# Kernel tuning notes

Measured on AMD Instinct MI355X. Metric: run time of the kernel, lower is better.

The kernel has to match this reference:

```python
import jax, jax.numpy as jnp
import numpy as np

N_NODES = 100000
N_EDGES = 1600000
IN_FEATS = 64
H_FEATS = 64
NUM_CLASSES = 32


def _cgnn(h, e, src, dst, W, b, n_nodes):
    # message: m = h[src] * e  (e is [E,1], broadcasts over feature dim)
    m = h[src] * e  # [E, F]
    # segment mean over destination nodes (DGL fn.mean -> 0 for isolated nodes)
    s = jax.ops.segment_sum(m, dst, num_segments=n_nodes)  # [N, F]
    deg = jax.ops.segment_sum(jnp.ones((m.shape[0],), m.dtype), dst,
                              num_segments=n_nodes)  # [N]
    h_N = s / jnp.maximum(deg, 1.0)[:, None]
    h_total = jnp.concatenate([h, h_N], axis=1)  # [N, 2F]
    return h_total @ W + b


def setup_inputs() -> dict:
    key = jax.random.key(0)
    k = jax.random.split(key, 8)
    in_feat = jax.random.normal(k[0], (N_NODES, IN_FEATS), dtype=jnp.float32)
    edge_feat = jax.random.uniform(k[1], (N_EDGES, 1), dtype=jnp.float32)
    src = jax.random.randint(k[2], (N_EDGES,), 0, N_NODES)
    dst = jax.random.randint(k[3], (N_EDGES,), 0, N_NODES)
    # Linear(2*in_feats, h_feats) and Linear(2*h_feats, num_classes)
    s1 = 1.0 / np.sqrt(2 * IN_FEATS)
    s2 = 1.0 / np.sqrt(2 * H_FEATS)
    W1 = jax.random.uniform(k[4], (2 * IN_FEATS, H_FEATS), jnp.float32, -s1, s1)
    b1 = jax.random.uniform(k[5], (H_FEATS,), jnp.float32, -s1, s1)
    W2 = jax.random.uniform(k[6], (2 * H_FEATS, NUM_CLASSES), jnp.float32, -s2, s2)
    b2 = jax.random.uniform(k[7], (NUM_CLASSES,), jnp.float32, -s2, s2)
    return {"in_feat": in_feat, "edge_feat": edge_feat, "src": src,
            "dst": dst, "W1": W1, "b1": b1, "W2": W2, "b2": b2}


def reference(in_feat, edge_feat, src, dst, W1, b1, W2, b2):
    h = _cgnn(in_feat, edge_feat, src, dst, W1, b1, N_NODES)
    h = jax.nn.relu(h)
    h = _cgnn(h, edge_feat, src, dst, W2, b2, N_NODES)
    return h
```

## Files before the change

kernel.cpp:

```cpp
#include <hip/hip_runtime.h>
#include <hip/hip_bf16.h>


#define F 64
#define EPT 8
#define TPB 1024
#define EPB (EPT * TPB)
#define SBSHIFT 8
#define SBSZ 256
#define NSBMAX 512
#define PADSB 4864

__global__ __launch_bounds__(256) void init_cursor_kernel(
    int* __restrict__ bcursor, int nsb)
{
    const int i = blockIdx.x * 256 + threadIdx.x;
    if (i < nsb) bcursor[i] = i * PADSB;
}

__global__ __launch_bounds__(TPB) void multisplit_kernel(
    const int* __restrict__ src, const int* __restrict__ dst,
    const float* __restrict__ ef, int* __restrict__ bcursor,
    int2* __restrict__ brec, int n_edges, int nsb)
{
    __shared__ int lcnt[NSBMAX];
    __shared__ int lbase[NSBMAX];
    const int tid = threadIdx.x;
    for (int i = tid; i < nsb; i += TPB) lcnt[i] = 0;
    __syncthreads();

    const int e0 = blockIdx.x * EPB + tid;
    int d[EPT], rk[EPT];
#pragma unroll
    for (int k = 0; k < EPT; ++k) {
        const int e = e0 + k * TPB;
        const int dd = (e < n_edges) ? dst[e] : -1;
        d[k]  = dd;
        rk[k] = (dd >= 0) ? atomicAdd(&lcnt[dd >> SBSHIFT], 1) : 0;
    }
    __syncthreads();
    for (int i = tid; i < nsb; i += TPB) {
        const int c = lcnt[i];
        lbase[i] = c ? atomicAdd(&bcursor[i], c) : 0;
    }
    __syncthreads();
#pragma unroll
    for (int k = 0; k < EPT; ++k) {
        const int e = e0 + k * TPB;
        if (e < n_edges) {
            const int dd  = d[k];
            const int bkt = dd >> SBSHIFT;
            const int pos = lbase[bkt] + rk[k];
            if (pos < (bkt + 1) * PADSB)
                brec[pos] = make_int2(((dd & (SBSZ - 1)) << 17) | src[e],
                                      __float_as_int(ef[e]));
        }
    }
}

__global__ __launch_bounds__(512) void bucket_sort_kernel(
    int2* __restrict__ brec, const int* __restrict__ bcursor,
    int* __restrict__ off2, int* __restrict__ end2,
    float* __restrict__ invdeg, int n_nodes)
{
    __shared__ int2 stage[PADSB];
    __shared__ int  lcnt[SBSZ];
    __shared__ int  lcur[SBSZ];
    __shared__ int  wsum[4];

    const int b   = blockIdx.x;
    const int tid = threadIdx.x;
    const int w0  = b * PADSB;
    int cnt = bcursor[b] - w0;
    if (cnt > PADSB) cnt = PADSB;

    if (tid < SBSZ) lcnt[tid] = 0;
    __syncthreads();

    for (int i = tid; i < cnt; i += 512) {
        const int2 r = brec[w0 + i];
        stage[i] = r;
        atomicAdd(&lcnt[r.x >> 17], 1);
    }
    __syncthreads();

    int v = 0, c = 0;
    if (tid < SBSZ) {
        c = lcnt[tid];
        v = c;
        for (int d = 1; d < 64; d <<= 1) {
            int t = __shfl_up(v, d, 64);
            if ((tid & 63) >= d) v += t;
        }
        if ((tid & 63) == 63) wsum[tid >> 6] = v;
    }
    __syncthreads();
    if (tid == 0) {
        int a = 0;
#pragma unroll
        for (int i = 0; i < 4; ++i) { int t = wsum[i]; wsum[i] = a; a += t; }
    }
    __syncthreads();
    if (tid < SBSZ) {
        const int excl = wsum[tid >> 6] + (v - c);
        lcur[tid] = excl;
        const int node = (b << SBSHIFT) + tid;
        if (node < n_nodes) {
            off2[node]   = w0 + excl;
            end2[node]   = w0 + excl + c;
            invdeg[node] = 1.0f / fmaxf((float)c, 1.0f);
        }
    }
    __syncthreads();

    for (int i = tid; i < cnt; i += 512) {
        const int2 r   = stage[i];
        const int  pos = atomicAdd(&lcur[r.x >> 17], 1);
        brec[w0 + pos] = make_int2((r.x & 0x1FFFF) << 7, r.y);
    }
}

__device__ __forceinline__ unsigned bf16_rne(float f)
{
    unsigned u = __float_as_uint(f);
    return (u + 0x7FFFu + ((u >> 16) & 1u)) >> 16;
}

__global__ __launch_bounds__(256) void f32_to_bf16_kernel(
    const float* __restrict__ x, unsigned short* __restrict__ y, int n8)
{
    const int i = blockIdx.x * 256 + threadIdx.x;
    if (i >= n8) return;
    const float4 a = ((const float4*)x)[2 * i];
    const float4 b = ((const float4*)x)[2 * i + 1];
    uint4 o;
    o.x = bf16_rne(a.x) | (bf16_rne(a.y) << 16);
    o.y = bf16_rne(a.z) | (bf16_rne(a.w) << 16);
    o.z = bf16_rne(b.x) | (bf16_rne(b.y) << 16);
    o.w = bf16_rne(b.z) | (bf16_rne(b.w) << 16);
    ((uint4*)y)[i] = o;
}

__global__ __launch_bounds__(256) void agg_kernel(
    const unsigned short* __restrict__ hb, const int2* __restrict__ rec,
    const int* __restrict__ off, const int* __restrict__ end,
    const float* __restrict__ invdeg, float* __restrict__ s, int n_nodes)
{
    const int wid  = (blockIdx.x * 256 + threadIdx.x) >> 6;
    const int lane = threadIdx.x & 63;
    const int n    = lane >> 5;
    const int r    = lane & 31;
    const int g    = r >> 3;
    const int q    = r & 7;

    const int  node   = wid * 2 + n;
    const bool active = node < n_nodes;
    const int  e0 = active ? off[node] : 0;
    const int  e1 = active ? end[node] : 0;

    const char* __restrict__ hq = (const char*)hb + q * 16;

    float4 aA0 = make_float4(0.f, 0.f, 0.f, 0.f);
    float4 aA1 = make_float4(0.f, 0.f, 0.f, 0.f);
    float4 aB0 = make_float4(0.f, 0.f, 0.f, 0.f);
    float4 aB1 = make_float4(0.f, 0.f, 0.f, 0.f);

    for (int base = e0; base < e1; base += 8) {
        const int  eA = base + g;
        const int  eB = base + 4 + g;
        const bool vA = eA < e1;
        const bool vB = eB < e1;
        const int2 rA = rec[vA ? eA : e0];
        const int2 rB = rec[vB ? eB : e0];
        const float evA = vA ? __int_as_float(rA.y) : 0.f;
        const float evB = vB ? __int_as_float(rB.y) : 0.f;
        const uint4 xA = *(const uint4*)(hq + rA.x);
        const uint4 xB = *(const uint4*)(hq + rB.x);

        aA0.x = fmaf(__uint_as_float(xA.x << 16),         evA, aA0.x);
        aA0.y = fmaf(__uint_as_float(xA.x & 0xFFFF0000u), evA, aA0.y);
        aA0.z = fmaf(__uint_as_float(xA.y << 16),         evA, aA0.z);
        aA0.w = fmaf(__uint_as_float(xA.y & 0xFFFF0000u), evA, aA0.w);
        aA1.x = fmaf(__uint_as_float(xA.z << 16),         evA, aA1.x);
        aA1.y = fmaf(__uint_as_float(xA.z & 0xFFFF0000u), evA, aA1.y);
        aA1.z = fmaf(__uint_as_float(xA.w << 16),         evA, aA1.z);
        aA1.w = fmaf(__uint_as_float(xA.w & 0xFFFF0000u), evA, aA1.w);

        aB0.x = fmaf(__uint_as_float(xB.x << 16),         evB, aB0.x);
        aB0.y = fmaf(__uint_as_float(xB.x & 0xFFFF0000u), evB, aB0.y);
        aB0.z = fmaf(__uint_as_float(xB.y << 16),         evB, aB0.z);
        aB0.w = fmaf(__uint_as_float(xB.y & 0xFFFF0000u), evB, aB0.w);
        aB1.x = fmaf(__uint_as_float(xB.z << 16),         evB, aB1.x);
        aB1.y = fmaf(__uint_as_float(xB.z & 0xFFFF0000u), evB, aB1.y);
        aB1.z = fmaf(__uint_as_float(xB.w << 16),         evB, aB1.z);
        aB1.w = fmaf(__uint_as_float(xB.w & 0xFFFF0000u), evB, aB1.w);
    }

    float4 a0 = make_float4(aA0.x + aB0.x, aA0.y + aB0.y,
                            aA0.z + aB0.z, aA0.w + aB0.w);
    float4 a1 = make_float4(aA1.x + aB1.x, aA1.y + aB1.y,
                            aA1.z + aB1.z, aA1.w + aB1.w);

#pragma unroll
    for (int m = 8; m <= 16; m <<= 1) {
        a0.x += __shfl_xor(a0.x, m); a0.y += __shfl_xor(a0.y, m);
        a0.z += __shfl_xor(a0.z, m); a0.w += __shfl_xor(a0.w, m);
        a1.x += __shfl_xor(a1.x, m); a1.y += __shfl_xor(a1.y, m);
        a1.z += __shfl_xor(a1.z, m); a1.w += __shfl_xor(a1.w, m);
    }

    if (g == 0 && active) {
        const float id = invdeg[node];
        float* __restrict__ srow = s + (size_t)node * F + q * 8;
        *(float4*)srow = make_float4(a0.x * id, a0.y * id, a0.z * id, a0.w * id);
        *(float4*)(srow + 4) = make_float4(a1.x * id, a1.y * id, a1.z * id, a1.w * id);
    }
}

template <int OUT, bool RELU, bool IN_BF16, bool OUT_BF16>
__global__ __launch_bounds__(256) void linear_lds_kernel(
    const float* __restrict__ hin_f, const unsigned short* __restrict__ hin_b,
    const float* __restrict__ s,
    const float* __restrict__ W, const float* __restrict__ b,
    float* __restrict__ out, unsigned short* __restrict__ hb_out, int n_nodes)
{
    constexpr int JT  = OUT / 4;
    constexpr int STR = 132;
    __shared__ float xin[64 * STR];

    const int tid   = threadIdx.x;
    const int node0 = blockIdx.x * 64;

    if constexpr (IN_BF16) {
        for (int i = tid; i < 512; i += 256) {
            const int ln = i >> 3, c8 = i & 7;
            const int node = node0 + ln;
            uint4 v = make_uint4(0u, 0u, 0u, 0u);
            if (node < n_nodes)
                v = *(const uint4*)&hin_b[(size_t)node * F + c8 * 8];
            float4 lo = make_float4(__uint_as_float(v.x << 16),
                                    __uint_as_float(v.x & 0xFFFF0000u),
                                    __uint_as_float(v.y << 16),
                                    __uint_as_float(v.y & 0xFFFF0000u));
            float4 hi = make_float4(__uint_as_float(v.z << 16),
                                    __uint_as_float(v.z & 0xFFFF0000u),
                                    __uint_as_float(v.w << 16),
                                    __uint_as_float(v.w & 0xFFFF0000u));
            *(float4*)&xin[ln * STR + c8 * 8]     = lo;
            *(float4*)&xin[ln * STR + c8 * 8 + 4] = hi;
        }
    } else {
        for (int i = tid; i < 1024; i += 256) {
            const int ln = i >> 4, c4 = i & 15;
            const int node = node0 + ln;
            float4 v = make_float4(0.f, 0.f, 0.f, 0.f);
            if (node < n_nodes)
                v = *(const float4*)&hin_f[(size_t)node * F + c4 * 4];
            *(float4*)&xin[ln * STR + c4 * 4] = v;
        }
    }
    for (int i = tid; i < 1024; i += 256) {
        const int ln = i >> 4, c4 = i & 15;
        const int node = node0 + ln;
        float4 v = make_float4(0.f, 0.f, 0.f, 0.f);
        if (node < n_nodes) v = *(const float4*)&s[(size_t)node * F + c4 * 4];
        *(float4*)&xin[ln * STR + F + c4 * 4] = v;
    }
    __syncthreads();

    const int lane = tid & 63;
    const int j0   = __builtin_amdgcn_readfirstlane((tid >> 6) * JT);

    float acc[JT];
#pragma unroll
    for (int j = 0; j < JT; ++j) acc[j] = b[j0 + j];

    const float* __restrict__ xrow = &xin[lane * STR];
#pragma unroll 2
    for (int k4 = 0; k4 < 32; ++k4) {
        const float4 xv = *(const float4*)&xrow[k4 * 4];
#pragma unroll
        for (int kk = 0; kk < 4; ++kk) {
            const int   k  = k4 * 4 + kk;
            const float xk = ((const float*)&xv)[kk];
#pragma unroll
            for (int j = 0; j < JT; ++j)
                acc[j] = fmaf(xk, W[k * OUT + j0 + j], acc[j]);
        }
    }

    const int node = node0 + lane;
    if (node < n_nodes) {
#pragma unroll
        for (int j = 0; j < JT; ++j) {
            float v = acc[j];
            if (RELU) v = fmaxf(v, 0.f);
            acc[j] = v;
        }
        if constexpr (OUT_BF16) {
            unsigned* __restrict__ hw =
                (unsigned*)(hb_out + (size_t)node * OUT + j0);
#pragma unroll
            for (int j = 0; j < JT; j += 2)
                hw[j >> 1] = bf16_rne(acc[j]) | (bf16_rne(acc[j + 1]) << 16);
        } else {
#pragma unroll
            for (int j = 0; j < JT; ++j)
                out[(size_t)node * OUT + j0 + j] = acc[j];
        }
    }
}

extern "C" void kernel_launch(void* const* d_in, const int* in_sizes, int n_in,
                              void* d_out, int out_size, void* d_ws, size_t ws_size,
                              hipStream_t stream)
{
    const float* in_feat   = (const float*)d_in[0];
    const float* edge_feat = (const float*)d_in[1];
    const int*   src       = (const int*)d_in[2];
    const int*   dst       = (const int*)d_in[3];
    const float* W1        = (const float*)d_in[4];
    const float* b1        = (const float*)d_in[5];
    const float* W2        = (const float*)d_in[6];
    const float* b2        = (const float*)d_in[7];
    float*       out       = (float*)d_out;

    const int n_nodes = in_sizes[0] / F;
    const int n_edges = in_sizes[2];
    const int nsb     = (n_nodes + SBSZ - 1) >> SBSHIFT;

    const int S = 100352;
    int*   wsi     = (int*)d_ws;
    int*   bcursor = wsi;
    int*   off2    = wsi + 1024;
    int*   end2    = wsi + 1024 + S;
    float* invdeg  = (float*)(wsi + 1024 + 2 * S);
    int2*  brec    = (int2*)(wsi + 1024 + 3 * S);
    float* s       = (float*)(brec + (size_t)nsb * PADSB);
    unsigned short* hb = (unsigned short*)(s + (size_t)n_nodes * F);

    const int egrid = (n_edges + EPB - 1) / EPB;
    init_cursor_kernel<<<(nsb + 255) / 256, 256, 0, stream>>>(bcursor, nsb);
    multisplit_kernel<<<egrid, TPB, 0, stream>>>(src, dst, edge_feat,
                                                 bcursor, brec, n_edges, nsb);
    bucket_sort_kernel<<<nsb, 512, 0, stream>>>(brec, bcursor, off2, end2,
                                                invdeg, n_nodes);

    const int n8    = (n_nodes * F) >> 3;
    const int cgrid = (n8 + 255) / 256;
    const int agrid = (n_nodes + 7) / 8;
    const int lgrid = (n_nodes + 63) / 64;

    f32_to_bf16_kernel<<<cgrid, 256, 0, stream>>>(in_feat, hb, n8);
    agg_kernel<<<agrid, 256, 0, stream>>>(hb, brec, off2, end2, invdeg, s, n_nodes);
    linear_lds_kernel<64, true, false, true><<<lgrid, 256, 0, stream>>>(
        in_feat, nullptr, s, W1, b1, nullptr, hb, n_nodes);

    agg_kernel<<<agrid, 256, 0, stream>>>(hb, brec, off2, end2, invdeg, s, n_nodes);
    linear_lds_kernel<32, false, true, false><<<lgrid, 256, 0, stream>>>(
        nullptr, hb, s, W2, b2, out, nullptr, n_nodes);
}
```

Before: 167.0 us.

## Store aggregates in bf16, fuse conversion with cursor init, unroll aggregation loop

```diff
diff --git a/kernel.cpp b/kernel.cpp
--- a/kernel.cpp
+++ b/kernel.cpp
@@ -11,11 +11,27 @@
 #define NSBMAX 512
 #define PADSB 4864
 
-__global__ __launch_bounds__(256) void init_cursor_kernel(
+__device__ __forceinline__ unsigned bf16_rne(float f)
+{
+    unsigned u = __float_as_uint(f);
+    return (u + 0x7FFFu + ((u >> 16) & 1u)) >> 16;
+}
+
+__global__ __launch_bounds__(256) void cvt_init_kernel(
+    const float* __restrict__ x, unsigned short* __restrict__ y, int n8,
     int* __restrict__ bcursor, int nsb)
 {
     const int i = blockIdx.x * 256 + threadIdx.x;
     if (i < nsb) bcursor[i] = i * PADSB;
+    if (i >= n8) return;
+    const float4 a = ((const float4*)x)[2 * i];
+    const float4 b = ((const float4*)x)[2 * i + 1];
+    uint4 o;
+    o.x = bf16_rne(a.x) | (bf16_rne(a.y) << 16);
+    o.y = bf16_rne(a.z) | (bf16_rne(a.w) << 16);
+    o.z = bf16_rne(b.x) | (bf16_rne(b.y) << 16);
+    o.w = bf16_rne(b.z) | (bf16_rne(b.w) << 16);
+    ((uint4*)y)[i] = o;
 }
 
 __global__ __launch_bounds__(TPB) void multisplit_kernel(
@@ -120,31 +136,11 @@
     }
 }
 
-__device__ __forceinline__ unsigned bf16_rne(float f)
-{
-    unsigned u = __float_as_uint(f);
-    return (u + 0x7FFFu + ((u >> 16) & 1u)) >> 16;
-}
-
-__global__ __launch_bounds__(256) void f32_to_bf16_kernel(
-    const float* __restrict__ x, unsigned short* __restrict__ y, int n8)
-{
-    const int i = blockIdx.x * 256 + threadIdx.x;
-    if (i >= n8) return;
-    const float4 a = ((const float4*)x)[2 * i];
-    const float4 b = ((const float4*)x)[2 * i + 1];
-    uint4 o;
-    o.x = bf16_rne(a.x) | (bf16_rne(a.y) << 16);
-    o.y = bf16_rne(a.z) | (bf16_rne(a.w) << 16);
-    o.z = bf16_rne(b.x) | (bf16_rne(b.y) << 16);
-    o.w = bf16_rne(b.z) | (bf16_rne(b.w) << 16);
-    ((uint4*)y)[i] = o;
-}
-
 __global__ __launch_bounds__(256) void agg_kernel(
     const unsigned short* __restrict__ hb, const int2* __restrict__ rec,
     const int* __restrict__ off, const int* __restrict__ end,
-    const float* __restrict__ invdeg, float* __restrict__ s, int n_nodes)
+    const float* __restrict__ invdeg, unsigned short* __restrict__ sb,
+    int n_nodes)
 {
     const int wid  = (blockIdx.x * 256 + threadIdx.x) >> 6;
     const int lane = threadIdx.x & 63;
@@ -164,42 +160,55 @@
     float4 aA1 = make_float4(0.f, 0.f, 0.f, 0.f);
     float4 aB0 = make_float4(0.f, 0.f, 0.f, 0.f);
     float4 aB1 = make_float4(0.f, 0.f, 0.f, 0.f);
-
-    for (int base = e0; base < e1; base += 8) {
+    float4 aC0 = make_float4(0.f, 0.f, 0.f, 0.f);
+    float4 aC1 = make_float4(0.f, 0.f, 0.f, 0.f);
+    float4 aD0 = make_float4(0.f, 0.f, 0.f, 0.f);
+    float4 aD1 = make_float4(0.f, 0.f, 0.f, 0.f);
+
+    for (int base = e0; base < e1; base += 16) {
         const int  eA = base + g;
         const int  eB = base + 4 + g;
-        const bool vA = eA < e1;
-        const bool vB = eB < e1;
+        const int  eC = base + 8 + g;
+        const int  eD = base + 12 + g;
+        const bool vA = eA < e1, vB = eB < e1, vC = eC < e1, vD = eD < e1;
         const int2 rA = rec[vA ? eA : e0];
         const int2 rB = rec[vB ? eB : e0];
+        const int2 rC = rec[vC ? eC : e0];
+        const int2 rD = rec[vD ? eD : e0];
         const float evA = vA ? __int_as_float(rA.y) : 0.f;
         const float evB = vB ? __int_as_float(rB.y) : 0.f;
+        const float evC = vC ? __int_as_float(rC.y) : 0.f;
+        const float evD = vD ? __int_as_float(rD.y) : 0.f;
         const uint4 xA = *(const uint4*)(hq + rA.x);
         const uint4 xB = *(const uint4*)(hq + rB.x);
-
-        aA0.x = fmaf(__uint_as_float(xA.x << 16),         evA, aA0.x);
-        aA0.y = fmaf(__uint_as_float(xA.x & 0xFFFF0000u), evA, aA0.y);
-        aA0.z = fmaf(__uint_as_float(xA.y << 16),         evA, aA0.z);
-        aA0.w = fmaf(__uint_as_float(xA.y & 0xFFFF0000u), evA, aA0.w);
-        aA1.x = fmaf(__uint_as_float(xA.z << 16),         evA, aA1.x);
-        aA1.y = fmaf(__uint_as_float(xA.z & 0xFFFF0000u), evA, aA1.y);
-        aA1.z = fmaf(__uint_as_float(xA.w << 16),         evA, aA1.z);
-        aA1.w = fmaf(__uint_as_float(xA.w & 0xFFFF0000u), evA, aA1.w);
-
-        aB0.x = fmaf(__uint_as_float(xB.x << 16),         evB, aB0.x);
-        aB0.y = fmaf(__uint_as_float(xB.x & 0xFFFF0000u), evB, aB0.y);
-        aB0.z = fmaf(__uint_as_float(xB.y << 16),         evB, aB0.z);
-        aB0.w = fmaf(__uint_as_float(xB.y & 0xFFFF0000u), evB, aB0.w);
-        aB1.x = fmaf(__uint_as_float(xB.z << 16),         evB, aB1.x);
-        aB1.y = fmaf(__uint_as_float(xB.z & 0xFFFF0000u), evB, aB1.y);
-        aB1.z = fmaf(__uint_as_float(xB.w << 16),         evB, aB1.z);
-        aB1.w = fmaf(__uint_as_float(xB.w & 0xFFFF0000u), evB, aB1.w);
-    }
-
-    float4 a0 = make_float4(aA0.x + aB0.x, aA0.y + aB0.y,
-                            aA0.z + aB0.z, aA0.w + aB0.w);
-    float4 a1 = make_float4(aA1.x + aB1.x, aA1.y + aB1.y,
-                            aA1.z + aB1.z, aA1.w + aB1.w);
+        const uint4 xC = *(const uint4*)(hq + rC.x);
+        const uint4 xD = *(const uint4*)(hq + rD.x);
+
+#define ACC8(xa, ev, lo, hi)                                         \
+        lo.x = fmaf(__uint_as_float(xa.x << 16),         ev, lo.x);  \
+        lo.y = fmaf(__uint_as_float(xa.x & 0xFFFF0000u), ev, lo.y);  \
+        lo.z = fmaf(__uint_as_float(xa.y << 16),         ev, lo.z);  \
+        lo.w = fmaf(__uint_as_float(xa.y & 0xFFFF0000u), ev, lo.w);  \
+        hi.x = fmaf(__uint_as_float(xa.z << 16),         ev, hi.x);  \
+        hi.y = fmaf(__uint_as_float(xa.z & 0xFFFF0000u), ev, hi.y);  \
+        hi.z = fmaf(__uint_as_float(xa.w << 16),         ev, hi.z);  \
+        hi.w = fmaf(__uint_as_float(xa.w & 0xFFFF0000u), ev, hi.w);
+
+        ACC8(xA, evA, aA0, aA1)
+        ACC8(xB, evB, aB0, aB1)
+        ACC8(xC, evC, aC0, aC1)
+        ACC8(xD, evD, aD0, aD1)
+#undef ACC8
+    }
+
+    float4 a0 = make_float4((aA0.x + aB0.x) + (aC0.x + aD0.x),
+                            (aA0.y + aB0.y) + (aC0.y + aD0.y),
+                            (aA0.z + aB0.z) + (aC0.z + aD0.z),
+                            (aA0.w + aB0.w) + (aC0.w + aD0.w));
+    float4 a1 = make_float4((aA1.x + aB1.x) + (aC1.x + aD1.x),
+                            (aA1.y + aB1.y) + (aC1.y + aD1.y),
+                            (aA1.z + aB1.z) + (aC1.z + aD1.z),
+                            (aA1.w + aB1.w) + (aC1.w + aD1.w));
 
 #pragma unroll
     for (int m = 8; m <= 16; m <<= 1) {
@@ -211,16 +220,19 @@
 
     if (g == 0 && active) {
         const float id = invdeg[node];
-        float* __restrict__ srow = s + (size_t)node * F + q * 8;
-        *(float4*)srow = make_float4(a0.x * id, a0.y * id, a0.z * id, a0.w * id);
-        *(float4*)(srow + 4) = make_float4(a1.x * id, a1.y * id, a1.z * id, a1.w * id);
-    }
-}
-
-template <int OUT, bool RELU, bool IN_BF16, bool OUT_BF16>
+        uint4 o;
+        o.x = bf16_rne(a0.x * id) | (bf16_rne(a0.y * id) << 16);
+        o.y = bf16_rne(a0.z * id) | (bf16_rne(a0.w * id) << 16);
+        o.z = bf16_rne(a1.x * id) | (bf16_rne(a1.y * id) << 16);
+        o.w = bf16_rne(a1.z * id) | (bf16_rne(a1.w * id) << 16);
+        *(uint4*)(sb + (size_t)node * F + q * 8) = o;
+    }
+}
+
+template <int OUT, bool RELU, bool OUT_BF16>
 __global__ __launch_bounds__(256) void linear_lds_kernel(
-    const float* __restrict__ hin_f, const unsigned short* __restrict__ hin_b,
-    const float* __restrict__ s,
+    const unsigned short* __restrict__ hin_b,
+    const unsigned short* __restrict__ sb,
     const float* __restrict__ W, const float* __restrict__ b,
     float* __restrict__ out, unsigned short* __restrict__ hb_out, int n_nodes)
 {
@@ -231,41 +243,28 @@
     const int tid   = threadIdx.x;
     const int node0 = blockIdx.x * 64;
 
-    if constexpr (IN_BF16) {
-        for (int i = tid; i < 512; i += 256) {
-            const int ln = i >> 3, c8 = i & 7;
-            const int node = node0 + ln;
-            uint4 v = make_uint4(0u, 0u, 0u, 0u);
-            if (node < n_nodes)
-                v = *(const uint4*)&hin_b[(size_t)node * F + c8 * 8];
-            float4 lo = make_float4(__uint_as_float(v.x << 16),
-                                    __uint_as_float(v.x & 0xFFFF0000u),
-                                    __uint_as_float(v.y << 16),
-                                    __uint_as_float(v.y & 0xFFFF0000u));
-            float4 hi = make_float4(__uint_as_float(v.z << 16),
-                                    __uint_as_float(v.z & 0xFFFF0000u),
-                                    __uint_as_float(v.w << 16),
-                                    __uint_as_float(v.w & 0xFFFF0000u));
-            *(float4*)&xin[ln * STR + c8 * 8]     = lo;
-            *(float4*)&xin[ln * STR + c8 * 8 + 4] = hi;
-        }
-    } else {
-        for (int i = tid; i < 1024; i += 256) {
-            const int ln = i >> 4, c4 = i & 15;
-            const int node = node0 + ln;
-            float4 v = make_float4(0.f, 0.f, 0.f, 0.f);
-            if (node < n_nodes)
-                v = *(const float4*)&hin_f[(size_t)node * F + c4 * 4];
-            *(float4*)&xin[ln * STR + c4 * 4] = v;
-        }
-    }
-    for (int i = tid; i < 1024; i += 256) {
-        const int ln = i >> 4, c4 = i & 15;
-        const int node = node0 + ln;
-        float4 v = make_float4(0.f, 0.f, 0.f, 0.f);
-        if (node < n_nodes) v = *(const float4*)&s[(size_t)node * F + c4 * 4];
-        *(float4*)&xin[ln * STR + F + c4 * 4] = v;
-    }
+#define STAGE_BF16(srcp, base_off)                                        \
+    for (int i = tid; i < 512; i += 256) {                                \
+        const int ln = i >> 3, c8 = i & 7;                                \
+        const int node = node0 + ln;                                     \
+        uint4 v = make_uint4(0u, 0u, 0u, 0u);                             \
+        if (node < n_nodes)                                               \
+            v = *(const uint4*)&srcp[(size_t)node * F + c8 * 8];          \
+        float4 lo = make_float4(__uint_as_float(v.x << 16),               \
+                                __uint_as_float(v.x & 0xFFFF0000u),       \
+                                __uint_as_float(v.y << 16),               \
+                                __uint_as_float(v.y & 0xFFFF0000u));      \
+        float4 hi = make_float4(__uint_as_float(v.z << 16),               \
+                                __uint_as_float(v.z & 0xFFFF0000u),       \
+                                __uint_as_float(v.w << 16),               \
+                                __uint_as_float(v.w & 0xFFFF0000u));      \
+        *(float4*)&xin[ln * STR + (base_off) + c8 * 8]     = lo;          \
+        *(float4*)&xin[ln * STR + (base_off) + c8 * 8 + 4] = hi;          \
+    }
+
+    STAGE_BF16(hin_b, 0)
+    STAGE_BF16(sb,    F)
+#undef STAGE_BF16
     __syncthreads();
 
     const int lane = tid & 63;
@@ -336,27 +335,27 @@
     int*   end2    = wsi + 1024 + S;
     float* invdeg  = (float*)(wsi + 1024 + 2 * S);
     int2*  brec    = (int2*)(wsi + 1024 + 3 * S);
-    float* s       = (float*)(brec + (size_t)nsb * PADSB);
-    unsigned short* hb = (unsigned short*)(s + (size_t)n_nodes * F);
-
+    unsigned short* sb  = (unsigned short*)(brec + (size_t)nsb * PADSB);
+    unsigned short* hb0 = sb  + (size_t)n_nodes * F;
+    unsigned short* hb1 = hb0 + (size_t)n_nodes * F;
+
+    const int n8    = (n_nodes * F) >> 3;
+    const int cgrid = (n8 + 255) / 256;
     const int egrid = (n_edges + EPB - 1) / EPB;
-    init_cursor_kernel<<<(nsb + 255) / 256, 256, 0, stream>>>(bcursor, nsb);
+    const int agrid = (n_nodes + 7) / 8;
+    const int lgrid = (n_nodes + 63) / 64;
+
+    cvt_init_kernel<<<cgrid, 256, 0, stream>>>(in_feat, hb0, n8, bcursor, nsb);
     multisplit_kernel<<<egrid, TPB, 0, stream>>>(src, dst, edge_feat,
                                                  bcursor, brec, n_edges, nsb);
     bucket_sort_kernel<<<nsb, 512, 0, stream>>>(brec, bcursor, off2, end2,
                                                 invdeg, n_nodes);
 
-    const int n8    = (n_nodes * F) >> 3;
-    const int cgrid = (n8 + 255) / 256;
-    const int agrid = (n_nodes + 7) / 8;
-    const int lgrid = (n_nodes + 63) / 64;
-
-    f32_to_bf16_kernel<<<cgrid, 256, 0, stream>>>(in_feat, hb, n8);
-    agg_kernel<<<agrid, 256, 0, stream>>>(hb, brec, off2, end2, invdeg, s, n_nodes);
-    linear_lds_kernel<64, true, false, true><<<lgrid, 256, 0, stream>>>(
-        in_feat, nullptr, s, W1, b1, nullptr, hb, n_nodes);
-
-    agg_kernel<<<agrid, 256, 0, stream>>>(hb, brec, off2, end2, invdeg, s, n_nodes);
-    linear_lds_kernel<32, false, true, false><<<lgrid, 256, 0, stream>>>(
-        nullptr, hb, s, W2, b2, out, nullptr, n_nodes);
-}
+    agg_kernel<<<agrid, 256, 0, stream>>>(hb0, brec, off2, end2, invdeg, sb, n_nodes);
+    linear_lds_kernel<64, true, true><<<lgrid, 256, 0, stream>>>(
+        hb0, sb, W1, b1, nullptr, hb1, n_nodes);
+
+    agg_kernel<<<agrid, 256, 0, stream>>>(hb1, brec, off2, end2, invdeg, sb, n_nodes);
+    linear_lds_kernel<32, false, false><<<lgrid, 256, 0, stream>>>(
+        hb1, sb, W2, b2, out, nullptr, n_nodes);
+}
```

Result: faster. 163.2 us (-2.3%).
